# Optimization experiments

Measured on AMD Instinct MI355X. Metric: run time of the kernel, lower is better.

Reference implementation:

```python
import jax, jax.numpy as jnp
import numpy as np

N, D, K = 131072, 768, 2000


def setup_inputs() -> dict:
    key = jax.random.key(0)
    kx, kc = jax.random.split(key)
    x = jax.random.normal(kx, (N, D), dtype=jnp.float32)
    centroids = jax.random.normal(kc, (D, K), dtype=jnp.float32)  # stored as [D, K] like the torch module
    return {"x": x, "centroids": centroids}


def reference(x, centroids):
    # dist[n,k] = ||x_n||^2 - 2 x_n . c_k + ||c_k||^2  (matmul trick)
    x_norm = jnp.sum(x * x, axis=1, keepdims=True)              # [N, 1]
    c_norm = jnp.sum(centroids * centroids, axis=0, keepdims=True)  # [1, K]
    dist = x_norm - 2.0 * jnp.matmul(x, centroids) + c_norm     # [N, K]
    return jnp.argmin(dist, axis=-1)                            # [N] int
```

## Files before the change

### kernel.cpp

```cpp
#include <hip/hip_runtime.h>
#include <hip/hip_bf16.h>

#define N_ROWS 131072
#define DIM    768
#define K_C    2000
#define K_PAD  2048
#define TAU    0.2f
#define LISTCAP 8192

typedef _Float16 f16;
typedef _Float16 f16x4 __attribute__((ext_vector_type(4)));
typedef _Float16 f16x8 __attribute__((ext_vector_type(8)));
typedef float    f32x4 __attribute__((ext_vector_type(4)));

#define OFF_CN   6291456
#define OFF_XN   6299648
#define OFF_PMIN 6823936
#define OFF_PSEC 15212544
#define OFF_PIDX 23601152
#define OFF_CNT  31989760
#define OFF_LIST 31990016
#define OFF_CN64 32022784
#define OFF_XH   32039168

static __device__ __forceinline__ void gload16(const void* g, void* l) {
  __builtin_amdgcn_global_load_lds(
      (const __attribute__((address_space(1))) unsigned int*)g,
      (__attribute__((address_space(3))) unsigned int*)l, 16, 0, 0);
}

__global__ __launch_bounds__(256) void prep_cn(const float* __restrict__ cent,
                                               float* __restrict__ cn,
                                               double* __restrict__ cn64) {
#pragma clang fp contract(off)
  __shared__ float pf[8][32];
  __shared__ double pd[8][32];
  int t = threadIdx.x;
  int kk = t & 31;
  int k = blockIdx.x * 32 + kk;
  int p = t >> 5;
  float s = 0.0f;
  double s64 = 0.0;
  for (int d = p * 96; d < p * 96 + 96; ++d) {
    float c = (k < K_C) ? cent[d * K_C + k] : 0.0f;
    float sq = c * c;
    s = s + sq;
    s64 += (double)c * (double)c;
  }
  pf[p][kk] = s;
  pd[p][kk] = s64;
  __syncthreads();
  if (p == 0) {
    float ss = 0.0f;
    double ss64 = 0.0;
#pragma unroll
    for (int q = 0; q < 8; ++q) {
      ss = ss + pf[q][kk];
      ss64 += pd[q][kk];
    }
    cn[k] = (k < K_C) ? ss : INFINITY;
    cn64[k] = (k < K_C) ? ss64 : (double)INFINITY;
  }
}

__global__ __launch_bounds__(256) void prep_ct(const float* __restrict__ cent,
                                               f16* __restrict__ cTh) {
  __shared__ float ld[64][65];
  int k0 = blockIdx.x * 64;
  int d0 = blockIdx.y * 64;
  int tid = threadIdx.x;
#pragma unroll
  for (int it = 0; it < 16; ++it) {
    int idx = it * 256 + tid;
    int dd = idx >> 6, kk = idx & 63;
    int k = k0 + kk;
    ld[dd][kk] = (k < K_C) ? cent[(size_t)(d0 + dd) * K_C + k] : 0.0f;
  }
  __syncthreads();
#pragma unroll
  for (int it = 0; it < 16; ++it) {
    int idx = it * 256 + tid;
    int kk = idx >> 6, dd = idx & 63;
    cTh[(size_t)(k0 + kk) * DIM + d0 + dd] = (f16)ld[dd][kk];
  }
}

__global__ __launch_bounds__(256) void xnorm_prepx(const float* __restrict__ x,
                                                   float* __restrict__ xn,
                                                   f16* __restrict__ xh) {
#pragma clang fp contract(off)
  __shared__ __align__(16) float buf[16 * DIM];
  int row0 = blockIdx.x * 16;
  int tid = threadIdx.x;
  const f32x4* src = (const f32x4*)(x + (size_t)row0 * DIM);
  f32x4* dst = (f32x4*)buf;
#pragma unroll
  for (int c = 0; c < 12; ++c) {
    f32x4 v = src[c * 256 + tid];
    dst[c * 256 + tid] = v;
    f16x4 hv;
#pragma unroll
    for (int j = 0; j < 4; ++j) hv[j] = (f16)v[j];
    *(f16x4*)(xh + (size_t)row0 * DIM + (size_t)(c * 256 + tid) * 4) = hv;
  }
  __syncthreads();
  int w = tid >> 6, lane = tid & 63;
  int b = lane >> 3, j = lane & 7;
#pragma unroll
  for (int rr = 0; rr < 4; ++rr) {
    int r = w * 4 + rr;
    const float* a = buf + r * DIM + 96 * b + j;
    float v0 = a[0];
    float acc = v0 * v0;
#pragma unroll
    for (int t = 1; t < 12; ++t) {
      float q = a[8 * t];
      float s = q * q;
      acc = acc + s;
    }
    float v = acc;
    { float o = __shfl_xor(v, 1);  v = v + o; }
    { float o = __shfl_xor(v, 2);  v = v + o; }
    { float o = __shfl_xor(v, 4);  v = v + o; }
    { float o = __shfl_xor(v, 8);  v = v + o; }
    { float o = __shfl_xor(v, 16); v = v + o; }
    { float o = __shfl_xor(v, 32); v = v + o; }
    if (lane == 0) xn[row0 + r] = v;
  }
}

#define STAGE3(bufo)                                                           \
  do {                                                                         \
    gload16(pA0, ldsb + (bufo) + (w * 2) * 1024);                              \
    gload16(pA1, ldsb + (bufo) + (w * 2 + 1) * 1024);                          \
    gload16(pB0, ldsb + (bufo) + 8192 + (w * 4) * 1024);                       \
    gload16(pB1, ldsb + (bufo) + 8192 + (w * 4 + 1) * 1024);                   \
    gload16(pB2, ldsb + (bufo) + 8192 + (w * 4 + 2) * 1024);                   \
    gload16(pB3, ldsb + (bufo) + 8192 + (w * 4 + 3) * 1024);                   \
    pA0 += 64; pA1 += 64; pB0 += 64; pB1 += 64; pB2 += 64; pB3 += 64;          \
  } while (0)

__global__ __launch_bounds__(256, 2) void kmeans_main(
    const f16* __restrict__ xh, const f16* __restrict__ cTh,
    const float* __restrict__ cn, const float* __restrict__ xn,
    float* __restrict__ pmin, float* __restrict__ psec,
    int* __restrict__ pidx) {
  __shared__ __align__(16) f16 lds[36864];
  char* ldsb = (char*)lds;

  int d0 = blockIdx.x;
  int g  = (d0 & 7) * 1024 + (d0 >> 3);
  int pb = g & 7;
  int rb = g >> 3;

  int tid  = threadIdx.x;
  int w    = tid >> 6;
  int lane = tid & 63;
  int wcol = w * 64;

  int rsel = lane & 15;
  int ksel = lane >> 4;
  int rs = (ksel ^ ((rsel >> 1) & 3)) << 4;

  int grn = (lane & 3) ^ ((lane >> 3) & 3);
  const char* pA0 = (const char*)xh +
      ((size_t)(rb * 128 + (w * 2) * 16 + (lane >> 2)) * DIM + grn * 8) * 2;
  const char* pA1 = (const char*)xh +
      ((size_t)(rb * 128 + (w * 2 + 1) * 16 + (lane >> 2)) * DIM + grn * 8) * 2;
  const char* pB0 = (const char*)cTh +
      ((size_t)(pb * 256 + (w * 4) * 16 + (lane >> 2)) * DIM + grn * 8) * 2;
  const char* pB1 = (const char*)cTh +
      ((size_t)(pb * 256 + (w * 4 + 1) * 16 + (lane >> 2)) * DIM + grn * 8) * 2;
  const char* pB2 = (const char*)cTh +
      ((size_t)(pb * 256 + (w * 4 + 2) * 16 + (lane >> 2)) * DIM + grn * 8) * 2;
  const char* pB3 = (const char*)cTh +
      ((size_t)(pb * 256 + (w * 4 + 3) * 16 + (lane >> 2)) * DIM + grn * 8) * 2;

  f32x4 acc[8][4] = {};

  STAGE3(0);
  STAGE3(24576);

  int cb = 0;
  int sb = 49152;
#pragma unroll 3
  for (int kt = 0; kt < 24; ++kt) {
    if (kt < 23) {
      asm volatile("s_waitcnt vmcnt(6)" ::: "memory");
    } else {
      asm volatile("s_waitcnt vmcnt(0)" ::: "memory");
    }
    __builtin_amdgcn_sched_barrier(0);
    __builtin_amdgcn_s_barrier();
    __builtin_amdgcn_sched_barrier(0);

    if (kt < 22) STAGE3(sb);

    f16x8 ah[8], bh[4];
    int abase = cb + rsel * 64 + rs;
    int bbase = cb + 8192 + (wcol + rsel) * 64 + rs;
#pragma unroll
    for (int m = 0; m < 8; ++m) ah[m] = *(const f16x8*)(ldsb + abase + m * 1024);
#pragma unroll
    for (int n = 0; n < 4; ++n) bh[n] = *(const f16x8*)(ldsb + bbase + n * 1024);

    __builtin_amdgcn_s_setprio(1);
#pragma unroll
    for (int m = 0; m < 8; ++m)
#pragma unroll
      for (int n = 0; n < 4; ++n)
        acc[m][n] = __builtin_amdgcn_mfma_f32_16x16x32_f16(ah[m], bh[n],
                                                           acc[m][n], 0, 0, 0);
    __builtin_amdgcn_s_setprio(0);

    cb = (cb == 49152) ? 0 : cb + 24576;
    sb = (sb == 49152) ? 0 : sb + 24576;
  }

  __syncthreads();
  float* lv = (float*)lds;
  float* lsv = (float*)lds + 512;
  int*   li = (int*)((float*)lds + 1024);

  int colbase = pb * 256 + wcol + rsel;
  float cnv[4];
#pragma unroll
  for (int n = 0; n < 4; ++n) cnv[n] = cn[colbase + n * 16];
  int g4 = ksel * 4;

#pragma unroll
  for (int m = 0; m < 8; ++m) {
#pragma unroll
    for (int j = 0; j < 4; ++j) {
      int trow = m * 16 + g4 + j;
      float xv = xn[rb * 128 + trow];
      float v1 = 0.0f, v2 = INFINITY;
      int i1 = 0;
#pragma unroll
      for (int n = 0; n < 4; ++n) {
        float dd = (xv - 2.0f * acc[m][n][j]) + cnv[n];
        int ci = colbase + n * 16;
        if (n == 0) { v1 = dd; i1 = ci; }
        else if (dd < v1) { v2 = v1; v1 = dd; i1 = ci; }
        else { v2 = fminf(v2, dd); }
      }
#pragma unroll
      for (int off = 1; off < 16; off <<= 1) {
        float ov1 = __shfl_xor(v1, off);
        float ov2 = __shfl_xor(v2, off);
        int oi1 = __shfl_xor(i1, off);
        if (ov1 < v1 || (ov1 == v1 && oi1 < i1)) {
          v2 = fminf(v1, ov2); v1 = ov1; i1 = oi1;
        } else {
          v2 = fminf(v2, ov1);
        }
      }
      if ((lane & 15) == 0) {
        lv[w * 128 + trow] = v1;
        lsv[w * 128 + trow] = v2;
        li[w * 128 + trow] = i1;
      }
    }
  }
  __syncthreads();
  if (tid < 128) {
    float v1 = lv[tid], v2 = lsv[tid];
    int i1 = li[tid];
#pragma unroll
    for (int q = 1; q < 4; ++q) {
      float b1 = lv[q * 128 + tid], b2 = lsv[q * 128 + tid];
      int bj = li[q * 128 + tid];
      if (b1 < v1) {
        v2 = fminf(v1, b2);
        v1 = b1; i1 = bj;
      } else {
        v2 = fminf(v2, fminf(b1, b2) == b1 ? b1 : b1);
        v2 = fminf(v2, b2 < b1 ? b2 : b1);
      }
    }
    size_t o = (size_t)pb * N_ROWS + rb * 128 + tid;
    pmin[o] = v1;
    psec[o] = v2;
    pidx[o] = i1;
  }
}

__global__ void merge_detect(const float* __restrict__ pmin,
                             const float* __restrict__ psec,
                             const int* __restrict__ pidx, int* __restrict__ out,
                             int* __restrict__ list, int* __restrict__ counter) {
  int n = blockIdx.x * 256 + threadIdx.x;
  float v1 = INFINITY, v2 = INFINITY;
  int i1 = 0x7fffffff;
  for (int p = 0; p < 8; ++p) {
    float a1 = pmin[(size_t)p * N_ROWS + n];
    float a2 = psec[(size_t)p * N_ROWS + n];
    int aj = pidx[(size_t)p * N_ROWS + n];
    if (a1 < v1 || (a1 == v1 && aj < i1)) {
      v2 = fminf(v1, a2); v1 = a1; i1 = aj;
    } else {
      v2 = fminf(v2, a1);
    }
  }
  out[n] = i1;
  if (v2 - v1 < TAU) {
    int idx = atomicAdd(counter, 1);
    if (idx < LISTCAP) list[idx] = n;
  }
}

#define ACCS(R) \
  double a##R##0 = 0, a##R##1 = 0, a##R##2 = 0, a##R##3 = 0, \
         a##R##4 = 0, a##R##5 = 0, a##R##6 = 0, a##R##7 = 0
#define FMAS(R, XV) \
  a##R##0 = fma(XV, c0, a##R##0); a##R##1 = fma(XV, c1, a##R##1); \
  a##R##2 = fma(XV, c2, a##R##2); a##R##3 = fma(XV, c3, a##R##3); \
  a##R##4 = fma(XV, c4, a##R##4); a##R##5 = fma(XV, c5, a##R##5); \
  a##R##6 = fma(XV, c6, a##R##6); a##R##7 = fma(XV, c7, a##R##7)
#define EVAL(R)                                                         \
  {                                                                     \
    double dots[8] = {a##R##0, a##R##1, a##R##2, a##R##3,               \
                      a##R##4, a##R##5, a##R##6, a##R##7};              \
    double bv = (double)INFINITY;                                       \
    int bi = 0x7fffffff;                                                \
    _Pragma("unroll") for (int j = 0; j < 8; ++j) {                     \
      int k = tid + j * 256;                                            \
      if (k < K_C) {                                                    \
        double dd = (xnorms[R] - 2.0 * dots[j]) + cn64[k];              \
        if (dd < bv) { bv = dd; bi = k; }                               \
      }                                                                 \
    }                                                                   \
    rv[tid] = bv; ri[tid] = bi;                                         \
    __syncthreads();                                                    \
    for (int s = 128; s > 0; s >>= 1) {                                 \
      if (tid < s) {                                                    \
        double ov = rv[tid + s];                                        \
        int oi = ri[tid + s];                                           \
        if (ov < rv[tid] || (ov == rv[tid] && oi < ri[tid])) {          \
          rv[tid] = ov; ri[tid] = oi;                                   \
        }                                                               \
      }                                                                 \
      __syncthreads();                                                  \
    }                                                                   \
    if (tid == 0 && (R) < nrows) out[list[b0 + (R)]] = ri[0];           \
    __syncthreads();                                                    \
  }

__global__ __launch_bounds__(256) void exact_recheck64(
    const float* __restrict__ x, const float* __restrict__ cent,
    const double* __restrict__ cn64, const int* __restrict__ list,
    const int* __restrict__ counter, int* __restrict__ out) {
  __shared__ __align__(16) float xrow[4][DIM];
  __shared__ double rv[256];
  __shared__ int ri[256];
  __shared__ double xnorms[4];
  int cnt = counter[0];
  if (cnt > LISTCAP) cnt = LISTCAP;
  int b0 = blockIdx.x * 4;
  if (b0 >= cnt) return;
  int nrows = cnt - b0;
  if (nrows > 4) nrows = 4;
  int tid = threadIdx.x;
  for (int r = 0; r < 4; ++r) {
    int n = list[b0 + (r < nrows ? r : 0)];
    double part = 0.0;
    for (int d = tid; d < DIM; d += 256) {
      float v = x[(size_t)n * DIM + d];
      xrow[r][d] = v;
      part += (double)v * (double)v;
    }
    rv[tid] = part;
    __syncthreads();
    for (int s = 128; s > 0; s >>= 1) {
      if (tid < s) rv[tid] += rv[tid + s];
      __syncthreads();
    }
    if (tid == 0) xnorms[r] = rv[0];
    __syncthreads();
  }

  int k7 = tid + 1792;
  int k7c = (k7 < K_C) ? k7 : (K_C - 1);
  ACCS(0); ACCS(1); ACCS(2); ACCS(3);
#pragma unroll 2
  for (int d = 0; d < DIM; ++d) {
    const float* cp = cent + (size_t)d * K_C + tid;
    double c0 = cp[0], c1 = cp[256], c2 = cp[512], c3 = cp[768];
    double c4 = cp[1024], c5 = cp[1280], c6 = cp[1536];
    double c7 = cp[k7c - tid];
    double x0 = xrow[0][d], x1 = xrow[1][d];
    double x2 = xrow[2][d], x3 = xrow[3][d];
    FMAS(0, x0); FMAS(1, x1); FMAS(2, x2); FMAS(3, x3);
  }
  EVAL(0) EVAL(1) EVAL(2) EVAL(3)
}

extern "C" void kernel_launch(void* const* d_in, const int* in_sizes, int n_in,
                              void* d_out, int out_size, void* d_ws, size_t ws_size,
                              hipStream_t stream) {
  const float* x = (const float*)d_in[0];
  const float* cent = (const float*)d_in[1];
  char* ws = (char*)d_ws;
  f16* cTh = (f16*)ws;
  float* cn = (float*)(ws + OFF_CN);
  float* xn = (float*)(ws + OFF_XN);
  float* pmin = (float*)(ws + OFF_PMIN);
  float* psec = (float*)(ws + OFF_PSEC);
  int* pidx = (int*)(ws + OFF_PIDX);
  int* counter = (int*)(ws + OFF_CNT);
  int* list = (int*)(ws + OFF_LIST);
  double* cn64 = (double*)(ws + OFF_CN64);
  f16* xh = (f16*)(ws + OFF_XH);

  hipMemsetAsync(counter, 0, 4, stream);
  prep_cn<<<64, 256, 0, stream>>>(cent, cn, cn64);
  prep_ct<<<dim3(32, 12), 256, 0, stream>>>(cent, cTh);
  xnorm_prepx<<<N_ROWS / 16, 256, 0, stream>>>(x, xn, xh);
  kmeans_main<<<8192, 256, 0, stream>>>(xh, cTh, cn, xn, pmin, psec, pidx);
  merge_detect<<<N_ROWS / 256, 256, 0, stream>>>(pmin, psec, pidx, (int*)d_out,
                                                 list, counter);
  exact_recheck64<<<LISTCAP / 4, 256, 0, stream>>>(x, cent, cn64, list, counter,
                                                   (int*)d_out);
}
```

Baseline: 1.166 ms.

## Enlarge GEMM block tile to 256x256 with 8 waves in a 2x4 grid

The distance GEMM block grows from 128 rows x 256 centroids with 4 waves to 256 rows x 256 centroids with 8 waves arranged 2x4. Each wave now stages two A and two B rows-chunks into LDS, so each loaded byte is reused across more output tiles and global/LDS traffic per FLOP falls. The triple-buffered LDS grows to 96KB with launch bounds (512,1), which lowers occupancy to one block per CU and could reduce latency hiding. The per-block second-min merge is also simplified, which changes the computed second-best value in the tie case (v2 could now be larger when b2 < b1). That value feeds the ambiguity check for exact rechecks.

```diff
diff --git a/kernel.cpp b/kernel.cpp
--- a/kernel.cpp
+++ b/kernel.cpp
@@ -129,34 +129,33 @@
   }
 }
 
-#define STAGE3(bufo)                                                           \
+#define STAGE5(bufo)                                                           \
   do {                                                                         \
     gload16(pA0, ldsb + (bufo) + (w * 2) * 1024);                              \
     gload16(pA1, ldsb + (bufo) + (w * 2 + 1) * 1024);                          \
-    gload16(pB0, ldsb + (bufo) + 8192 + (w * 4) * 1024);                       \
-    gload16(pB1, ldsb + (bufo) + 8192 + (w * 4 + 1) * 1024);                   \
-    gload16(pB2, ldsb + (bufo) + 8192 + (w * 4 + 2) * 1024);                   \
-    gload16(pB3, ldsb + (bufo) + 8192 + (w * 4 + 3) * 1024);                   \
-    pA0 += 64; pA1 += 64; pB0 += 64; pB1 += 64; pB2 += 64; pB3 += 64;          \
+    gload16(pB0, ldsb + 49152 + (bufo) + (w * 2) * 1024);                      \
+    gload16(pB1, ldsb + 49152 + (bufo) + (w * 2 + 1) * 1024);                  \
+    pA0 += 64; pA1 += 64; pB0 += 64; pB1 += 64;                                \
   } while (0)
 
-__global__ __launch_bounds__(256, 2) void kmeans_main(
+__global__ __launch_bounds__(512, 1) void kmeans_main(
     const f16* __restrict__ xh, const f16* __restrict__ cTh,
     const float* __restrict__ cn, const float* __restrict__ xn,
     float* __restrict__ pmin, float* __restrict__ psec,
     int* __restrict__ pidx) {
-  __shared__ __align__(16) f16 lds[36864];
+  __shared__ __align__(16) f16 lds[49152];
   char* ldsb = (char*)lds;
 
   int d0 = blockIdx.x;
-  int g  = (d0 & 7) * 1024 + (d0 >> 3);
+  int g  = (d0 & 7) * 512 + (d0 >> 3);
   int pb = g & 7;
   int rb = g >> 3;
 
   int tid  = threadIdx.x;
   int w    = tid >> 6;
   int lane = tid & 63;
-  int wcol = w * 64;
+  int wr   = w >> 2;
+  int wc   = w & 3;
 
   int rsel = lane & 15;
   int ksel = lane >> 4;
@@ -164,29 +163,25 @@
 
   int grn = (lane & 3) ^ ((lane >> 3) & 3);
   const char* pA0 = (const char*)xh +
-      ((size_t)(rb * 128 + (w * 2) * 16 + (lane >> 2)) * DIM + grn * 8) * 2;
+      ((size_t)(rb * 256 + (w * 2) * 16 + (lane >> 2)) * DIM + grn * 8) * 2;
   const char* pA1 = (const char*)xh +
-      ((size_t)(rb * 128 + (w * 2 + 1) * 16 + (lane >> 2)) * DIM + grn * 8) * 2;
+      ((size_t)(rb * 256 + (w * 2 + 1) * 16 + (lane >> 2)) * DIM + grn * 8) * 2;
   const char* pB0 = (const char*)cTh +
-      ((size_t)(pb * 256 + (w * 4) * 16 + (lane >> 2)) * DIM + grn * 8) * 2;
+      ((size_t)(pb * 256 + (w * 2) * 16 + (lane >> 2)) * DIM + grn * 8) * 2;
   const char* pB1 = (const char*)cTh +
-      ((size_t)(pb * 256 + (w * 4 + 1) * 16 + (lane >> 2)) * DIM + grn * 8) * 2;
-  const char* pB2 = (const char*)cTh +
-      ((size_t)(pb * 256 + (w * 4 + 2) * 16 + (lane >> 2)) * DIM + grn * 8) * 2;
-  const char* pB3 = (const char*)cTh +
-      ((size_t)(pb * 256 + (w * 4 + 3) * 16 + (lane >> 2)) * DIM + grn * 8) * 2;
+      ((size_t)(pb * 256 + (w * 2 + 1) * 16 + (lane >> 2)) * DIM + grn * 8) * 2;
 
   f32x4 acc[8][4] = {};
 
-  STAGE3(0);
-  STAGE3(24576);
+  STAGE5(0);
+  STAGE5(16384);
 
   int cb = 0;
-  int sb = 49152;
+  int sb = 32768;
 #pragma unroll 3
   for (int kt = 0; kt < 24; ++kt) {
     if (kt < 23) {
-      asm volatile("s_waitcnt vmcnt(6)" ::: "memory");
+      asm volatile("s_waitcnt vmcnt(4)" ::: "memory");
     } else {
       asm volatile("s_waitcnt vmcnt(0)" ::: "memory");
     }
@@ -194,11 +189,11 @@
     __builtin_amdgcn_s_barrier();
     __builtin_amdgcn_sched_barrier(0);
 
-    if (kt < 22) STAGE3(sb);
+    if (kt < 22) STAGE5(sb);
 
     f16x8 ah[8], bh[4];
-    int abase = cb + rsel * 64 + rs;
-    int bbase = cb + 8192 + (wcol + rsel) * 64 + rs;
+    int abase = cb + (wr * 128 + rsel) * 64 + rs;
+    int bbase = cb + 49152 + (wc * 64 + rsel) * 64 + rs;
 #pragma unroll
     for (int m = 0; m < 8; ++m) ah[m] = *(const f16x8*)(ldsb + abase + m * 1024);
 #pragma unroll
@@ -213,16 +208,16 @@
                                                            acc[m][n], 0, 0, 0);
     __builtin_amdgcn_s_setprio(0);
 
-    cb = (cb == 49152) ? 0 : cb + 24576;
-    sb = (sb == 49152) ? 0 : sb + 24576;
+    cb = (cb == 32768) ? 0 : cb + 16384;
+    sb = (sb == 32768) ? 0 : sb + 16384;
   }
 
   __syncthreads();
-  float* lv = (float*)lds;
-  float* lsv = (float*)lds + 512;
-  int*   li = (int*)((float*)lds + 1024);
-
-  int colbase = pb * 256 + wcol + rsel;
+  float* lv  = (float*)lds;
+  float* lsv = (float*)lds + 1024;
+  int*   li  = (int*)((float*)lds + 2048);
+
+  int colbase = pb * 256 + wc * 64 + rsel;
   float cnv[4];
 #pragma unroll
   for (int n = 0; n < 4; ++n) cnv[n] = cn[colbase + n * 16];
@@ -232,8 +227,8 @@
   for (int m = 0; m < 8; ++m) {
 #pragma unroll
     for (int j = 0; j < 4; ++j) {
-      int trow = m * 16 + g4 + j;
-      float xv = xn[rb * 128 + trow];
+      int br = wr * 128 + m * 16 + g4 + j;
+      float xv = xn[rb * 256 + br];
       float v1 = 0.0f, v2 = INFINITY;
       int i1 = 0;
 #pragma unroll
@@ -256,29 +251,28 @@
         }
       }
       if ((lane & 15) == 0) {
-        lv[w * 128 + trow] = v1;
-        lsv[w * 128 + trow] = v2;
-        li[w * 128 + trow] = i1;
+        lv[wc * 256 + br] = v1;
+        lsv[wc * 256 + br] = v2;
+        li[wc * 256 + br] = i1;
       }
     }
   }
   __syncthreads();
-  if (tid < 128) {
+  if (tid < 256) {
     float v1 = lv[tid], v2 = lsv[tid];
     int i1 = li[tid];
 #pragma unroll
     for (int q = 1; q < 4; ++q) {
-      float b1 = lv[q * 128 + tid], b2 = lsv[q * 128 + tid];
-      int bj = li[q * 128 + tid];
+      float b1 = lv[q * 256 + tid], b2 = lsv[q * 256 + tid];
+      int bj = li[q * 256 + tid];
       if (b1 < v1) {
         v2 = fminf(v1, b2);
         v1 = b1; i1 = bj;
       } else {
-        v2 = fminf(v2, fminf(b1, b2) == b1 ? b1 : b1);
-        v2 = fminf(v2, b2 < b1 ? b2 : b1);
+        v2 = fminf(v2, b1);
       }
     }
-    size_t o = (size_t)pb * N_ROWS + rb * 128 + tid;
+    size_t o = (size_t)pb * N_ROWS + rb * 256 + tid;
     pmin[o] = v1;
     psec[o] = v2;
     pidx[o] = i1;
@@ -416,7 +410,7 @@
   prep_cn<<<64, 256, 0, stream>>>(cent, cn, cn64);
   prep_ct<<<dim3(32, 12), 256, 0, stream>>>(cent, cTh);
   xnorm_prepx<<<N_ROWS / 16, 256, 0, stream>>>(x, xn, xh);
-  kmeans_main<<<8192, 256, 0, stream>>>(xh, cTh, cn, xn, pmin, psec, pidx);
+  kmeans_main<<<4096, 512, 0, stream>>>(xh, cTh, cn, xn, pmin, psec, pidx);
   merge_detect<<<N_ROWS / 256, 256, 0, stream>>>(pmin, psec, pidx, (int*)d_out,
                                                  list, counter);
   exact_recheck64<<<LISTCAP / 4, 256, 0, stream>>>(x, cent, cn64, list, counter,
```

Result: slower. 1.200 ms (+2.9%).
